# Optimization experiments

Hardware: AMD Instinct MI355X
Metric: run time of the kernel (lower is better)

The kernel has to match this reference:

```python
import jax, jax.numpy as jnp
import numpy as np

# Llama-7B-like config with CPSVD split projections
B, S, H = 1, 1024, 4096
NH, HD = 32, 128          # num_heads, head_dim
RANK = 1024               # SVD rank per projection
NCOL = 512                # exactly-kept columns per projection
NSVD = H - NCOL           # SVD-compressed columns
ROPE_BASE = 10000.0
WSCALE = 0.02


def setup_inputs() -> dict:
    key = jax.random.key(0)
    ks = jax.random.split(key, 16)
    hidden_states = jax.random.normal(ks[0], (B, S, H), jnp.float32)
    # causal additive mask (large negative above diagonal)
    causal = jnp.triu(jnp.full((S, S), -1e9, jnp.float32), k=1)
    attention_mask = jnp.broadcast_to(causal, (B, 1, S, S))
    position_ids = jnp.broadcast_to(jnp.arange(S, dtype=jnp.int32), (B, S))
    # disjoint partition of the 4096 input columns: 512 kept, 3584 SVD'd
    col_idx = jnp.arange(0, H, H // NCOL, dtype=jnp.int32)          # [512]
    keep = np.ones(H, dtype=bool); keep[np.asarray(col_idx)] = False
    svd_idx = jnp.asarray(np.nonzero(keep)[0], dtype=jnp.int32)      # [3584]
    # per-projection weights (torch Linear convention: [out, in])
    def w(k, shape):
        return jax.random.normal(k, shape, jnp.float32) * WSCALE
    inp = dict(hidden_states=hidden_states, attention_mask=attention_mask,
               position_ids=position_ids, col_idx=col_idx, svd_idx=svd_idx)
    names = ['q', 'k', 'v', 'o']
    for i, p in enumerate(names):
        inp[f'{p}_v_w'] = w(ks[1 + 3 * i], (RANK, NSVD))   # v_proj: n_svd -> rank
        inp[f'{p}_u_w'] = w(ks[2 + 3 * i], (H, RANK))      # u_proj: rank -> hidden
        inp[f'{p}_col_w'] = w(ks[3 + 3 * i], (H, NCOL))    # col: n_col -> hidden
    return inp


def _split_proj(x, svd_idx, col_idx, v_w, u_w, col_w):
    # x: [B,S,H] -> gather + low-rank (V then U) + exact-column matmul, added
    x_svd = x[..., svd_idx]                                  # [B,S,NSVD]
    x_col = x[..., col_idx]                                  # [B,S,NCOL]
    low = jnp.einsum('bsr,hr->bsh', jnp.einsum('bsn,rn->bsr', x_svd, v_w), u_w)
    return low + jnp.einsum('bsc,hc->bsh', x_col, col_w)     # [B,S,H]


def _rotate_half(x):
    x1, x2 = x[..., : HD // 2], x[..., HD // 2 :]
    return jnp.concatenate((-x2, x1), axis=-1)


def reference(hidden_states, attention_mask, position_ids, col_idx, svd_idx,
              q_v_w, q_u_w, q_col_w, k_v_w, k_u_w, k_col_w,
              v_v_w, v_u_w, v_col_w, o_v_w, o_u_w, o_col_w):
    bsz, q_len, _ = hidden_states.shape

    def heads(t):  # [B,S,H] -> [B,NH,S,HD]
        return t.reshape(bsz, q_len, NH, HD).transpose(0, 2, 1, 3)

    q = heads(_split_proj(hidden_states, svd_idx, col_idx, q_v_w, q_u_w, q_col_w))
    k = heads(_split_proj(hidden_states, svd_idx, col_idx, k_v_w, k_u_w, k_col_w))
    v = heads(_split_proj(hidden_states, svd_idx, col_idx, v_v_w, v_u_w, v_col_w))

    # rotary embedding: direct indexed read of cos/sin tables
    inv_freq = 1.0 / (ROPE_BASE ** (jnp.arange(0, HD, 2, dtype=jnp.float32) / HD))
    ang = jnp.arange(q_len, dtype=jnp.float32)[:, None] * inv_freq[None, :]  # [S,HD/2]
    emb = jnp.concatenate((ang, ang), axis=-1)                               # [S,HD]
    cos = jnp.cos(emb)[position_ids][:, None, :, :]                          # [B,1,S,HD]
    sin = jnp.sin(emb)[position_ids][:, None, :, :]
    q = q * cos + _rotate_half(q) * sin
    k = k * cos + _rotate_half(k) * sin

    scale = 1.0 / jnp.sqrt(jnp.float32(HD))
    attn = jnp.einsum('bhqd,bhkd->bhqk', q, k) * scale
    attn = attn + attention_mask
    attn = jnp.maximum(attn, jnp.finfo(attn.dtype).min)
    attn = jax.nn.softmax(attn.astype(jnp.float32), axis=-1).astype(q.dtype)
    out = jnp.einsum('bhqk,bhkd->bhqd', attn, v)             # [B,NH,S,HD]
    out = out.transpose(0, 2, 1, 3).reshape(bsz, q_len, NH * HD)
    out = _split_proj(out, svd_idx, col_idx, o_v_w, o_u_w, o_col_w)
    return out
```

## Files before the change

### kernel.cpp

```cpp
#include <hip/hip_runtime.h>

typedef __attribute__((ext_vector_type(8))) short short8;
typedef __attribute__((ext_vector_type(4))) float f32x4;
typedef unsigned short u16;
typedef unsigned int u32;
typedef unsigned long long u64;

__device__ __forceinline__ u16 f2bf(float f) {
  u32 u = __builtin_bit_cast(u32, f);
  u32 r = u + 0x7FFFu + ((u >> 16) & 1u);
  return (u16)(r >> 16);
}
__device__ __forceinline__ float bf2f(u16 h) {
  u32 u = ((u32)h) << 16;
  return __builtin_bit_cast(float, u);
}
__device__ __forceinline__ u32 cvtpk(float lo, float hi) {
  u32 r;
  asm("v_cvt_pk_bf16_f32 %0, %1, %2" : "=v"(r) : "v"(lo), "v"(hi));
  return r;
}

__device__ __forceinline__ void gload16(const void* g, void* l) {
  __builtin_amdgcn_global_load_lds(
      (const __attribute__((address_space(1))) void*)(u64)g,
      (__attribute__((address_space(3))) void*)(u32)(u64)l,
      16, 0, 0);
}

__global__ void prep_w(const float* __restrict__ qv, const float* __restrict__ qu, const float* __restrict__ qc,
                       const float* __restrict__ kv, const float* __restrict__ ku, const float* __restrict__ kc,
                       const float* __restrict__ vv, const float* __restrict__ vu, const float* __restrict__ vc,
                       const float* __restrict__ ov, const float* __restrict__ ou, const float* __restrict__ oc,
                       u16* __restrict__ W1q, u16* __restrict__ W1o,
                       u16* __restrict__ W2q, u16* __restrict__ W2o) {
  long i = (long)blockIdx.x * 256 + threadIdx.x;
  if (i < 3670016L) {
    int which = (int)(i / 917504);
    int j = (int)(i % 917504);
    const float* src = which == 0 ? qv : which == 1 ? kv : which == 2 ? vv : ov;
    u16* dst = which < 3 ? W1q + (long)which * 3670016 : W1o;
    float4 v = ((const float4*)src)[j];
    ushort4 o;
    o.x = f2bf(v.x); o.y = f2bf(v.y); o.z = f2bf(v.z); o.w = f2bf(v.w);
    ((ushort4*)dst)[j] = o;
  } else {
    long j2 = i - 3670016L;
    int which = (int)(j2 / 1572864);
    int rem = (int)(j2 % 1572864);
    int r = rem / 384, c4 = rem % 384;
    const float* u = which == 0 ? qu : which == 1 ? ku : which == 2 ? vu : ou;
    const float* cc = which == 0 ? qc : which == 1 ? kc : which == 2 ? vc : oc;
    u16* dst = which < 3 ? W2q + (long)which * 6291456 : W2o;
    float4 v = (c4 < 256) ? ((const float4*)(u + (long)r * 1024))[c4]
                          : ((const float4*)(cc + (long)r * 512))[c4 - 256];
    ushort4 o;
    o.x = f2bf(v.x); o.y = f2bf(v.y); o.z = f2bf(v.z); o.w = f2bf(v.w);
    ((ushort4*)(dst + (long)r * 1536))[c4] = o;
  }
}

__global__ void gather_in(const float* __restrict__ hid, const int* __restrict__ svd,
                          const int* __restrict__ col, u16* __restrict__ Xs,
                          u16* __restrict__ X2) {
  int s = blockIdx.x;
  const float* row = hid + (long)s * 4096;
  for (int j = threadIdx.x; j < 3584; j += blockDim.x)
    Xs[(long)s * 3584 + j] = f2bf(row[svd[j]]);
  for (int c = threadIdx.x; c < 512; c += blockDim.x) {
    u16 v = f2bf(row[col[c]]);
    X2[(long)s * 1536 + 1024 + c] = v;
    X2[1024L * 1536 + (long)s * 1536 + 1024 + c] = v;
    X2[2 * 1024L * 1536 + (long)s * 1536 + 1024 + c] = v;
  }
}

__global__ void rope2(const u16* __restrict__ P, u16* __restrict__ Qh, u16* __restrict__ Kh) {
  int t = blockIdx.x * 256 + threadIdx.x;
  int which = t >> 21;
  int rem = t & 2097151;
  int d0 = rem & 63, s = (rem >> 6) & 1023, h = rem >> 16;
  const u16* src = P + (long)which * 4194304;
  float x1 = bf2f(src[(long)s * 4096 + h * 128 + d0]);
  float x2 = bf2f(src[(long)s * 4096 + h * 128 + d0 + 64]);
  float inv = exp2f(-(float)d0 * 0.20762050593046013f);
  float ang = (float)s * inv;
  float sn = __sinf(ang), cs = __cosf(ang);
  float scale = which ? 1.0f : (0.08838834764831845f * 1.44269504088896340f);
  u16* dst = which ? Kh : Qh;
  long o = ((long)h * 1024 + s) * 128 + d0;
  dst[o] = f2bf((x1 * cs - x2 * sn) * scale);
  dst[o + 64] = f2bf((x2 * cs + x1 * sn) * scale);
}

__global__ void vtrans(const u16* __restrict__ P, u16* __restrict__ Vt) {
  __shared__ u16 t[64][65];
  int h = blockIdx.z, d0 = blockIdx.y * 64, s0 = blockIdx.x * 64;
  int c = threadIdx.x & 63, r0 = threadIdx.x >> 6;
  for (int r = r0; r < 64; r += 4)
    t[r][c] = P[(long)(s0 + r) * 4096 + h * 128 + d0 + c];
  __syncthreads();
  for (int r = r0; r < 64; r += 4)
    Vt[(long)(h * 128 + d0 + r) * 1024 + s0 + c] = t[c][r];
}

template <int BM, int FOUT>
__global__ __launch_bounds__(256) void gemm_nt(const u16* __restrict__ A,
                                               const u16* __restrict__ B,
                                               void* __restrict__ Cv, int K, int ldc,
                                               long sAz, long sBz, long sCz) {
  __shared__ __align__(16) u16 As[BM * 64];
  __shared__ __align__(16) u16 Bs[128 * 64];
  constexpr int MF = BM / 32;
  const int tid = threadIdx.x;
  const int w = tid >> 6, lane = tid & 63;
  const int wr = w >> 1, wc = w & 1;
  const int lr = lane & 15, lk = lane >> 4;
  const u16* Ab = A + (long)blockIdx.z * sAz + (long)blockIdx.y * BM * K;
  const u16* Bb = B + (long)blockIdx.z * sBz + (long)blockIdx.x * 128 * K;
  const int srow = w * 8 + (lane >> 3);
  const int scol = (lane & 7) * 8;

  f32x4 acc[MF][4] = {};

  for (int k0 = 0; k0 < K; k0 += 64) {
#pragma unroll
    for (int i = 0; i < BM / 32; ++i)
      gload16(Ab + (long)(i * 32 + srow) * K + k0 + scol, &As[i * 2048 + w * 512]);
#pragma unroll
    for (int i = 0; i < 4; ++i)
      gload16(Bb + (long)(i * 32 + srow) * K + k0 + scol, &Bs[i * 2048 + w * 512]);
    __syncthreads();
#pragma unroll
    for (int kk = 0; kk < 2; ++kk) {
      short8 af[MF], bf[4];
#pragma unroll
      for (int m = 0; m < MF; ++m)
        af[m] = *(const short8*)&As[(wr * (BM / 2) + m * 16 + lr) * 64 + kk * 32 + lk * 8];
#pragma unroll
      for (int n = 0; n < 4; ++n)
        bf[n] = *(const short8*)&Bs[(wc * 64 + n * 16 + lr) * 64 + kk * 32 + lk * 8];
#pragma unroll
      for (int m = 0; m < MF; ++m)
#pragma unroll
        for (int n = 0; n < 4; ++n)
          acc[m][n] = __builtin_amdgcn_mfma_f32_16x16x32_bf16(af[m], bf[n], acc[m][n], 0, 0, 0);
    }
    __syncthreads();
  }

  const long crow = (long)blockIdx.y * BM + wr * (BM / 2) + lk * 4;
  const long ccol = (long)blockIdx.x * 128 + wc * 64 + lr;
  if constexpr (FOUT == 0) {
    u16* C = (u16*)Cv + (long)blockIdx.z * sCz;
#pragma unroll
    for (int m = 0; m < MF; ++m)
#pragma unroll
      for (int n = 0; n < 4; ++n)
#pragma unroll
        for (int j = 0; j < 4; ++j)
          C[(crow + m * 16 + j) * ldc + ccol + n * 16] = f2bf(acc[m][n][j]);
  } else {
    float* C = (float*)Cv + (long)blockIdx.z * sCz;
#pragma unroll
    for (int m = 0; m < MF; ++m)
#pragma unroll
      for (int n = 0; n < 4; ++n)
#pragma unroll
        for (int j = 0; j < 4; ++j)
          C[(crow + m * 16 + j) * ldc + ccol + n * 16] = acc[m][n][j];
  }
}

__global__ __launch_bounds__(256) void attn_k(const u16* __restrict__ Qh,
                                              const u16* __restrict__ Kh,
                                              const u16* __restrict__ Vt,
                                              u16* __restrict__ Xso,
                                              u16* __restrict__ X2o) {
  const int bid = blockIdx.x;
  const int xcd = bid & 7, t = bid >> 3;
  const int p = t & 15, hg = t >> 4;
  const int h = hg * 8 + xcd;
  const int w = threadIdx.x >> 6, lane = threadIdx.x & 63;
  const int lr = lane & 15, lk = lane >> 4;
  const int rh = w >> 1;

#pragma unroll
  for (int ph = 0; ph < 2; ++ph) {
    const int qt = ((w & 1) ^ ph) ? p : 31 - p;
    const int q0 = qt * 32 + rh * 16;
    const int ktmax = q0 >> 6;
    const u16* qp = &Qh[((long)h * 1024 + q0 + lr) * 128 + lk * 8];
    short8 qf[4];
#pragma unroll
    for (int kk = 0; kk < 4; ++kk) qf[kk] = *(const short8*)&qp[kk * 32];
    f32x4 oacc[8] = {};
    float lsum = 0.f;

    for (int kt = 0; kt <= ktmax; ++kt) {
      const int k0 = kt * 64;
      f32x4 sacc[4];
#pragma unroll
      for (int ct = 0; ct < 4; ++ct) {
        if (k0 + ct * 16 > q0 + 15) {
          sacc[ct] = f32x4{-3.0e38f, -3.0e38f, -3.0e38f, -3.0e38f};
        } else {
          f32x4 s = {};
          const u16* kp = &Kh[((long)h * 1024 + k0 + ct * 16 + lr) * 128 + lk * 8];
#pragma unroll
          for (int kk = 0; kk < 4; ++kk) {
            short8 kf = *(const short8*)&kp[kk * 32];
            s = __builtin_amdgcn_mfma_f32_16x16x32_bf16(kf, qf[kk], s, 0, 0, 0);
          }
          sacc[ct] = s;
        }
      }
      if (kt == ktmax) {
#pragma unroll
        for (int ct = 0; ct < 4; ++ct)
#pragma unroll
          for (int j = 0; j < 4; ++j)
            if (k0 + ct * 16 + lk * 4 + j > q0 + lr) sacc[ct][j] = -3.0e38f;
      }
#pragma unroll
      for (int ct = 0; ct < 4; ++ct)
#pragma unroll
        for (int j = 0; j < 4; ++j) {
          float pv = exp2f(sacc[ct][j]);
          sacc[ct][j] = pv;
          lsum += pv;
        }
      union U8 { short8 s; u32 u[4]; };
      U8 pf0, pf1;
      pf0.u[0] = cvtpk(sacc[0][0], sacc[0][1]); pf0.u[1] = cvtpk(sacc[0][2], sacc[0][3]);
      pf0.u[2] = cvtpk(sacc[1][0], sacc[1][1]); pf0.u[3] = cvtpk(sacc[1][2], sacc[1][3]);
      pf1.u[0] = cvtpk(sacc[2][0], sacc[2][1]); pf1.u[1] = cvtpk(sacc[2][2], sacc[2][3]);
      pf1.u[2] = cvtpk(sacc[3][0], sacc[3][1]); pf1.u[3] = cvtpk(sacc[3][2], sacc[3][3]);
#pragma unroll
      for (int dt = 0; dt < 8; ++dt) {
        const u16* vp = &Vt[((long)h * 128 + dt * 16 + lr) * 1024 + k0 + lk * 4];
        union U8 vf0, vf1;
        uint2 a0 = *(const uint2*)(vp);
        uint2 a1 = *(const uint2*)(vp + 16);
        uint2 b0 = *(const uint2*)(vp + 32);
        uint2 b1 = *(const uint2*)(vp + 48);
        vf0.u[0] = a0.x; vf0.u[1] = a0.y; vf0.u[2] = a1.x; vf0.u[3] = a1.y;
        vf1.u[0] = b0.x; vf1.u[1] = b0.y; vf1.u[2] = b1.x; vf1.u[3] = b1.y;
        oacc[dt] = __builtin_amdgcn_mfma_f32_16x16x32_bf16(pf0.s, vf0.s, oacc[dt], 0, 0, 0);
        oacc[dt] = __builtin_amdgcn_mfma_f32_16x16x32_bf16(pf1.s, vf1.s, oacc[dt], 0, 0, 0);
      }
    }

    lsum += __shfl_xor(lsum, 16);
    lsum += __shfl_xor(lsum, 32);
    float linv[4];
#pragma unroll
    for (int j = 0; j < 4; ++j) linv[j] = 1.f / __shfl(lsum, lk * 4 + j);
#pragma unroll
    for (int j = 0; j < 4; ++j) {
      const int q = q0 + lk * 4 + j;
#pragma unroll
      for (int dt = 0; dt < 8; ++dt) {
        const int H = h * 128 + dt * 16 + lr;
        u16 b = f2bf(oacc[dt][j] * linv[j]);
        if ((H & 7) == 0) X2o[(long)q * 1536 + 1024 + (H >> 3)] = b;
        else Xso[(long)q * 3584 + H - (H >> 3) - 1] = b;
      }
    }
  }
}

extern "C" void kernel_launch(void* const* d_in, const int* in_sizes, int n_in,
                              void* d_out, int out_size, void* d_ws, size_t ws_size,
                              hipStream_t stream) {
  (void)in_sizes; (void)n_in; (void)out_size; (void)ws_size;
  const float* hid = (const float*)d_in[0];
  const int* colI = (const int*)d_in[3];
  const int* svdI = (const int*)d_in[4];
  const float* W[12];
  for (int i = 0; i < 12; ++i) W[i] = (const float*)d_in[5 + i];

  char* ws = (char*)d_ws;
  u16* W1q = (u16*)(ws + 0);
  u16* W2q = (u16*)(ws + 22020096);
  u16* P   = (u16*)(ws + 59768832);
  u16* W1o = (u16*)(ws + 84934656);
  u16* W2o = (u16*)(ws + 92274688);
  u16* Xs  = (u16*)(ws + 104857600);
  u16* X2  = (u16*)(ws + 112197632);
  u16* Qh  = (u16*)(ws + 124780544);
  u16* Kh  = (u16*)(ws + 133169152);
  u16* Vt  = (u16*)(ws + 141557760);
  u16* Xso = (u16*)(ws + 149946368);
  u16* X2o = X2 + 3UL * 1024 * 1536;

  prep_w<<<38912, 256, 0, stream>>>(W[0], W[1], W[2], W[3], W[4], W[5],
                                    W[6], W[7], W[8], W[9], W[10], W[11],
                                    W1q, W1o, W2q, W2o);
  gather_in<<<1024, 256, 0, stream>>>(hid, svdI, colI, Xs, X2);

  gemm_nt<64, 0><<<dim3(8, 16, 3), 256, 0, stream>>>(Xs, W1q, X2, 3584, 1536, 0L,
                                                     1024L * 3584, 1024L * 1536);
  gemm_nt<128, 0><<<dim3(32, 8, 3), 256, 0, stream>>>(X2, W2q, P, 1536, 4096,
                                                      1024L * 1536, 4096L * 1536, 1024L * 4096);
  rope2<<<16384, 256, 0, stream>>>(P, Qh, Kh);
  vtrans<<<dim3(16, 2, 32), 256, 0, stream>>>(P + 2UL * 1024 * 4096, Vt);

  attn_k<<<512, 256, 0, stream>>>(Qh, Kh, Vt, Xso, X2o);

  gemm_nt<64, 0><<<dim3(8, 16, 1), 256, 0, stream>>>(Xso, W1o, X2o, 3584, 1536, 0L, 0L, 0L);
  gemm_nt<64, 1><<<dim3(32, 16, 1), 256, 0, stream>>>(X2o, W2o, d_out, 1536, 4096, 0L, 0L, 0L);
}
```

Before: 637.2 us.

## Split attention KV loop across warps and shrink GEMM N-tiles for occupancy

The attention kernel now runs 512 threads per block. Four warp groups each take every fourth KV tile of the same query tile, and their partial outputs and row sums are reduced through shared memory before normalisation and the scatter store. Skipping the max subtraction is what makes summing the partials valid. The GEMM template gains a BN parameter, and the first-stage and o-proj V GEMMs use 64-wide N tiles to double their block count. This trades extra shared-memory reduction, block-wide syncs and more redundant A-tile loads for more parallelism on the skinny GEMMs and in attention.

```diff
diff --git a/kernel.cpp b/kernel.cpp
--- a/kernel.cpp
+++ b/kernel.cpp
@@ -104,59 +104,60 @@
     Vt[(long)(h * 128 + d0 + r) * 1024 + s0 + c] = t[c][r];
 }
 
-template <int BM, int FOUT>
+template <int BM, int BN, int FOUT>
 __global__ __launch_bounds__(256) void gemm_nt(const u16* __restrict__ A,
                                                const u16* __restrict__ B,
                                                void* __restrict__ Cv, int K, int ldc,
                                                long sAz, long sBz, long sCz) {
   __shared__ __align__(16) u16 As[BM * 64];
-  __shared__ __align__(16) u16 Bs[128 * 64];
+  __shared__ __align__(16) u16 Bs[BN * 64];
   constexpr int MF = BM / 32;
+  constexpr int NF = BN / 32;
   const int tid = threadIdx.x;
   const int w = tid >> 6, lane = tid & 63;
   const int wr = w >> 1, wc = w & 1;
   const int lr = lane & 15, lk = lane >> 4;
   const u16* Ab = A + (long)blockIdx.z * sAz + (long)blockIdx.y * BM * K;
-  const u16* Bb = B + (long)blockIdx.z * sBz + (long)blockIdx.x * 128 * K;
+  const u16* Bb = B + (long)blockIdx.z * sBz + (long)blockIdx.x * BN * K;
   const int srow = w * 8 + (lane >> 3);
   const int scol = (lane & 7) * 8;
 
-  f32x4 acc[MF][4] = {};
+  f32x4 acc[MF][NF] = {};
 
   for (int k0 = 0; k0 < K; k0 += 64) {
 #pragma unroll
     for (int i = 0; i < BM / 32; ++i)
       gload16(Ab + (long)(i * 32 + srow) * K + k0 + scol, &As[i * 2048 + w * 512]);
 #pragma unroll
-    for (int i = 0; i < 4; ++i)
+    for (int i = 0; i < BN / 32; ++i)
       gload16(Bb + (long)(i * 32 + srow) * K + k0 + scol, &Bs[i * 2048 + w * 512]);
     __syncthreads();
 #pragma unroll
     for (int kk = 0; kk < 2; ++kk) {
-      short8 af[MF], bf[4];
+      short8 af[MF], bf[NF];
 #pragma unroll
       for (int m = 0; m < MF; ++m)
         af[m] = *(const short8*)&As[(wr * (BM / 2) + m * 16 + lr) * 64 + kk * 32 + lk * 8];
 #pragma unroll
-      for (int n = 0; n < 4; ++n)
-        bf[n] = *(const short8*)&Bs[(wc * 64 + n * 16 + lr) * 64 + kk * 32 + lk * 8];
+      for (int n = 0; n < NF; ++n)
+        bf[n] = *(const short8*)&Bs[(wc * (BN / 2) + n * 16 + lr) * 64 + kk * 32 + lk * 8];
 #pragma unroll
       for (int m = 0; m < MF; ++m)
 #pragma unroll
-        for (int n = 0; n < 4; ++n)
+        for (int n = 0; n < NF; ++n)
           acc[m][n] = __builtin_amdgcn_mfma_f32_16x16x32_bf16(af[m], bf[n], acc[m][n], 0, 0, 0);
     }
     __syncthreads();
   }
 
   const long crow = (long)blockIdx.y * BM + wr * (BM / 2) + lk * 4;
-  const long ccol = (long)blockIdx.x * 128 + wc * 64 + lr;
+  const long ccol = (long)blockIdx.x * BN + wc * (BN / 2) + lr;
   if constexpr (FOUT == 0) {
     u16* C = (u16*)Cv + (long)blockIdx.z * sCz;
 #pragma unroll
     for (int m = 0; m < MF; ++m)
 #pragma unroll
-      for (int n = 0; n < 4; ++n)
+      for (int n = 0; n < NF; ++n)
 #pragma unroll
         for (int j = 0; j < 4; ++j)
           C[(crow + m * 16 + j) * ldc + ccol + n * 16] = f2bf(acc[m][n][j]);
@@ -165,29 +166,31 @@
 #pragma unroll
     for (int m = 0; m < MF; ++m)
 #pragma unroll
-      for (int n = 0; n < 4; ++n)
+      for (int n = 0; n < NF; ++n)
 #pragma unroll
         for (int j = 0; j < 4; ++j)
           C[(crow + m * 16 + j) * ldc + ccol + n * 16] = acc[m][n][j];
   }
 }
 
-__global__ __launch_bounds__(256) void attn_k(const u16* __restrict__ Qh,
-                                              const u16* __restrict__ Kh,
-                                              const u16* __restrict__ Vt,
-                                              u16* __restrict__ Xso,
-                                              u16* __restrict__ X2o) {
+__global__ __launch_bounds__(512, 4) void attn_k(const u16* __restrict__ Qh,
+                                                 const u16* __restrict__ Kh,
+                                                 const u16* __restrict__ Vt,
+                                                 u16* __restrict__ Xso,
+                                                 u16* __restrict__ X2o) {
   const int bid = blockIdx.x;
-  const int xcd = bid & 7, t = bid >> 3;
-  const int p = t & 15, hg = t >> 4;
+  const int xcd = bid & 7, hg = (bid >> 3) & 3, p = bid >> 5;
   const int h = hg * 8 + xcd;
   const int w = threadIdx.x >> 6, lane = threadIdx.x & 63;
+  const int rh = w & 1, c = w >> 1;
   const int lr = lane & 15, lk = lane >> 4;
-  const int rh = w >> 1;
+
+  __shared__ float OB[4][2][16][132];
+  __shared__ float LB[4][2][16];
 
 #pragma unroll
   for (int ph = 0; ph < 2; ++ph) {
-    const int qt = ((w & 1) ^ ph) ? p : 31 - p;
+    const int qt = ph ? 31 - p : p;
     const int q0 = qt * 32 + rh * 16;
     const int ktmax = q0 >> 6;
     const u16* qp = &Qh[((long)h * 1024 + q0 + lr) * 128 + lk * 8];
@@ -197,7 +200,7 @@
     f32x4 oacc[8] = {};
     float lsum = 0.f;
 
-    for (int kt = 0; kt <= ktmax; ++kt) {
+    for (int kt = c; kt <= ktmax; kt += 4) {
       const int k0 = kt * 64;
       f32x4 sacc[4];
 #pragma unroll
@@ -253,20 +256,27 @@
 
     lsum += __shfl_xor(lsum, 16);
     lsum += __shfl_xor(lsum, 32);
-    float linv[4];
-#pragma unroll
-    for (int j = 0; j < 4; ++j) linv[j] = 1.f / __shfl(lsum, lk * 4 + j);
-#pragma unroll
-    for (int j = 0; j < 4; ++j) {
-      const int q = q0 + lk * 4 + j;
-#pragma unroll
-      for (int dt = 0; dt < 8; ++dt) {
-        const int H = h * 128 + dt * 16 + lr;
-        u16 b = f2bf(oacc[dt][j] * linv[j]);
-        if ((H & 7) == 0) X2o[(long)q * 1536 + 1024 + (H >> 3)] = b;
-        else Xso[(long)q * 3584 + H - (H >> 3) - 1] = b;
-      }
+    if (lk == 0) LB[c][rh][lr] = lsum;
+#pragma unroll
+    for (int dt = 0; dt < 8; ++dt)
+#pragma unroll
+      for (int j = 0; j < 4; ++j)
+        OB[c][rh][lk * 4 + j][dt * 16 + lr] = oacc[dt][j];
+    __syncthreads();
+
+    for (int e = threadIdx.x; e < 4096; e += 512) {
+      int d = e & 127, row = e >> 7;
+      int rh2 = row >> 4, r2 = row & 15;
+      float o = OB[0][rh2][r2][d] + OB[1][rh2][r2][d] +
+                OB[2][rh2][r2][d] + OB[3][rh2][r2][d];
+      float l = LB[0][rh2][r2] + LB[1][rh2][r2] + LB[2][rh2][r2] + LB[3][rh2][r2];
+      int q = qt * 32 + row;
+      int H = h * 128 + d;
+      u16 b = f2bf(o / l);
+      if ((H & 7) == 0) X2o[(long)q * 1536 + 1024 + (H >> 3)] = b;
+      else Xso[(long)q * 3584 + H - (H >> 3) - 1] = b;
     }
+    __syncthreads();
   }
 }
 
@@ -299,15 +309,18 @@
                                     W1q, W1o, W2q, W2o);
   gather_in<<<1024, 256, 0, stream>>>(hid, svdI, colI, Xs, X2);
 
-  gemm_nt<64, 0><<<dim3(8, 16, 3), 256, 0, stream>>>(Xs, W1q, X2, 3584, 1536, 0L,
-                                                     1024L * 3584, 1024L * 1536);
-  gemm_nt<128, 0><<<dim3(32, 8, 3), 256, 0, stream>>>(X2, W2q, P, 1536, 4096,
-                                                      1024L * 1536, 4096L * 1536, 1024L * 4096);
+  gemm_nt<64, 64, 0><<<dim3(16, 16, 3), 256, 0, stream>>>(Xs, W1q, X2, 3584, 1536, 0L,
+                                                          1024L * 3584, 1024L * 1536);
+  gemm_nt<128, 128, 0><<<dim3(32, 8, 3), 256, 0, stream>>>(X2, W2q, P, 1536, 4096,
+                                                           1024L * 1536, 4096L * 1536,
+                                                           1024L * 4096);
   rope2<<<16384, 256, 0, stream>>>(P, Qh, Kh);
   vtrans<<<dim3(16, 2, 32), 256, 0, stream>>>(P + 2UL * 1024 * 4096, Vt);
 
-  attn_k<<<512, 256, 0, stream>>>(Qh, Kh, Vt, Xso, X2o);
-
-  gemm_nt<64, 0><<<dim3(8, 16, 1), 256, 0, stream>>>(Xso, W1o, X2o, 3584, 1536, 0L, 0L, 0L);
-  gemm_nt<64, 1><<<dim3(32, 16, 1), 256, 0, stream>>>(X2o, W2o, d_out, 1536, 4096, 0L, 0L, 0L);
-}
+  attn_k<<<512, 512, 0, stream>>>(Qh, Kh, Vt, Xso, X2o);
+
+  gemm_nt<64, 64, 0><<<dim3(16, 16, 1), 256, 0, stream>>>(Xso, W1o, X2o, 3584, 1536,
+                                                          0L, 0L, 0L);
+  gemm_nt<64, 128, 1><<<dim3(32, 16, 1), 256, 0, stream>>>(X2o, W2o, d_out, 1536, 4096,
+                                                           0L, 0L, 0L);
+}
```

Measured after the change: 551.9 us. -13.4%, faster.
